# Kernel tuning notes

Measured on AMD Instinct MI355X. Metric: run time of the kernel, lower is better.

The kernel has to match this reference:

```python
import jax, jax.numpy as jnp
import numpy as np

B, S, E = 4, 2048, 1024
H = 16
D = E // H  # head_dim = 64


def setup_inputs() -> dict:
    key = jax.random.key(0)
    k1, k2, k3 = jax.random.split(key, 3)
    x = jax.random.normal(k1, (B, S, E), dtype=jnp.float32)
    w_qkv = jax.random.normal(k2, (E, 3 * E), dtype=jnp.float32) * (E ** -0.5)
    b_qkv = jnp.zeros((3 * E,), dtype=jnp.float32)
    w_proj = jax.random.normal(k3, (E, E), dtype=jnp.float32) * (E ** -0.5)
    b_proj = jnp.zeros((E,), dtype=jnp.float32)
    return {"x": x, "w_qkv": w_qkv, "b_qkv": b_qkv, "w_proj": w_proj, "b_proj": b_proj}


def reference(x, w_qkv, b_qkv, w_proj, b_proj):
    bsz, seq_len, emb = x.shape
    scale = D ** -0.5
    qkv = x @ w_qkv + b_qkv                      # [B,S,3E]
    q, k, v = jnp.split(qkv, 3, axis=2)
    # [B,S,E] -> [B,H,S,D]
    q = q.reshape(bsz, seq_len, H, D).transpose(0, 2, 1, 3)
    k = k.reshape(bsz, seq_len, H, D).transpose(0, 2, 1, 3)
    v = v.reshape(bsz, seq_len, H, D).transpose(0, 2, 1, 3)
    att = jnp.einsum('bhqd,bhkd->bhqk', q, k) * scale
    causal = jnp.tril(jnp.ones((seq_len, seq_len), dtype=bool))
    att = jnp.where(causal, att, -jnp.inf)
    att = jax.nn.softmax(att, axis=-1)
    y = jnp.einsum('bhqk,bhkd->bhqd', att, v)
    y = y.transpose(0, 2, 1, 3).reshape(bsz, seq_len, emb)
    return y @ w_proj + b_proj
```

## Files before the change

### kernel.cpp

```cpp
#include <hip/hip_runtime.h>
#include <hip/hip_bf16.h>
#include <stdint.h>

#define S_LEN 2048
#define EMB   1024
#define NH    16
#define HD    64

typedef unsigned short u16;
typedef __attribute__((ext_vector_type(2))) float f32x2;
typedef __attribute__((ext_vector_type(4))) float f32x4;
typedef __attribute__((ext_vector_type(8))) short bf16x8;

typedef __attribute__((address_space(1))) const unsigned char gas_t;
typedef __attribute__((address_space(3))) unsigned char las_t;

static __device__ __forceinline__ void gld_lds16(const void* g, void* l) {
  __builtin_amdgcn_global_load_lds((gas_t*)g, (las_t*)l, 16, 0, 0);
}

static __device__ __forceinline__ u16 f2bf(float f) {
  unsigned int u = __builtin_bit_cast(unsigned int, f);
  u = u + 0x7fffu + ((u >> 16) & 1u);
  return (u16)(u >> 16);
}

static __device__ __forceinline__ float fexp2(float x) {
  float r;
  asm("v_exp_f32 %0, %1" : "=v"(r) : "v"(x));
  return r;
}

static __device__ __forceinline__ unsigned cvt_pk_bf16(float lo, float hi) {
  unsigned r;
  asm("v_cvt_pk_bf16_f32 %0, %1, %2" : "=v"(r) : "v"(lo), "v"(hi));
  return r;
}

static __device__ __forceinline__ float max3(float a, float b, float c) {
  float r;
  asm("v_max3_f32 %0, %1, %2, %3" : "=v"(r) : "v"(a), "v"(b), "v"(c));
  return r;
}

static __device__ __forceinline__ f32x2 pk_add(f32x2 a, f32x2 b) {
  f32x2 r;
  asm("v_pk_add_f32 %0, %1, %2" : "=v"(r) : "v"(a), "v"(b));
  return r;
}
static __device__ __forceinline__ f32x2 pk_mul(f32x2 a, f32x2 b) {
  f32x2 r;
  asm("v_pk_mul_f32 %0, %1, %2" : "=v"(r) : "v"(a), "v"(b));
  return r;
}
static __device__ __forceinline__ f32x2 pk_fma(f32x2 a, f32x2 b, f32x2 c) {
  f32x2 r;
  asm("v_pk_fma_f32 %0, %1, %2, %3" : "=v"(r) : "v"(a), "v"(b), "v"(c));
  return r;
}
#define HALF0(v) __builtin_shufflevector(v, v, 0, 1)
#define HALF1(v) __builtin_shufflevector(v, v, 2, 3)

static __device__ __forceinline__ float red4rows_max(float x) {
  unsigned u = __builtin_bit_cast(unsigned, x);
  auto r = __builtin_amdgcn_permlane32_swap(u, u, false, false);
  float y = fmaxf(__builtin_bit_cast(float, (unsigned)r[0]),
                  __builtin_bit_cast(float, (unsigned)r[1]));
  unsigned v = __builtin_bit_cast(unsigned, y);
  auto r2 = __builtin_amdgcn_permlane16_swap(v, v, false, false);
  return fmaxf(__builtin_bit_cast(float, (unsigned)r2[0]),
               __builtin_bit_cast(float, (unsigned)r2[1]));
}
static __device__ __forceinline__ float red4rows_sum(float x) {
  unsigned u = __builtin_bit_cast(unsigned, x);
  auto r = __builtin_amdgcn_permlane32_swap(u, u, false, false);
  float y = __builtin_bit_cast(float, (unsigned)r[0]) +
            __builtin_bit_cast(float, (unsigned)r[1]);
  unsigned v = __builtin_bit_cast(unsigned, y);
  auto r2 = __builtin_amdgcn_permlane16_swap(v, v, false, false);
  return __builtin_bit_cast(float, (unsigned)r2[0]) +
         __builtin_bit_cast(float, (unsigned)r2[1]);
}

__global__ __launch_bounds__(256) void k_prep(const float* __restrict__ x,
                                              u16* __restrict__ xb,
                                              const float* __restrict__ w_qkv,
                                              u16* __restrict__ wqkvT,
                                              const float* __restrict__ w_proj,
                                              u16* __restrict__ wprojT) {
  __shared__ u16 tile[64][68];
  const int bid = blockIdx.x;
  const int t = threadIdx.x;
  if (bid < 1024) {
    const int n4 = (8192 * 1024) / 4;
    int i = bid * 256 + t;
    for (; i < n4; i += 1024 * 256) {
      float4 f = ((const float4*)x)[i];
      ushort4 o;
      o.x = f2bf(f.x); o.y = f2bf(f.y); o.z = f2bf(f.z); o.w = f2bf(f.w);
      ((ushort4*)xb)[i] = o;
    }
    return;
  }
  const float* W;
  u16* WT;
  int c0, r0, K, N;
  if (bid < 1792) {
    const int idx = bid - 1024;
    W = w_qkv; WT = wqkvT; K = 1024; N = 3072;
    c0 = (idx % 48) * 64; r0 = (idx / 48) * 64;
  } else {
    const int idx = bid - 1792;
    W = w_proj; WT = wprojT; K = 1024; N = 1024;
    c0 = (idx & 15) * 64; r0 = (idx >> 4) * 64;
  }
  const int tr = t >> 4, tc4 = (t & 15) * 4;
#pragma unroll
  for (int i = 0; i < 4; i++) {
    const int r = tr + 16 * i;
    float4 f = *(const float4*)&W[(size_t)(r0 + r) * N + c0 + tc4];
    ushort4 o;
    o.x = f2bf(f.x); o.y = f2bf(f.y); o.z = f2bf(f.z); o.w = f2bf(f.w);
    *(ushort4*)&tile[r][tc4] = o;
  }
  __syncthreads();
  const int oc = t >> 2, or0 = (t & 3) * 16;
  u16 vals[16];
#pragma unroll
  for (int j = 0; j < 16; j++) vals[j] = tile[or0 + j][oc];
  u16* dst = &WT[(size_t)(c0 + oc) * K + r0 + or0];
  *(uint4*)dst = *(const uint4*)&vals[0];
  *(uint4*)(dst + 8) = *(const uint4*)&vals[8];
}

template <int MODE>
__global__ __launch_bounds__(256) void k_gemm(const u16* __restrict__ A,
                                              const u16* __restrict__ BT,
                                              const float* __restrict__ bias,
                                              float* __restrict__ Cout,
                                              u16* __restrict__ q_ws,
                                              u16* __restrict__ k_ws,
                                              u16* __restrict__ v_t,
                                              int N, int K) {
  __shared__ u16 As[2][128 * 32];
  __shared__ u16 Bs[2][128 * 32];
  const int tid = threadIdx.x;
  const int w = tid >> 6, lane = tid & 63;
  const int wr = w >> 1, wc = w & 1;
  const int lrow = lane & 15, lk8 = (lane >> 4) * 8;
  const int orig = blockIdx.y * gridDim.x + blockIdx.x;
  const int total = gridDim.x * gridDim.y;
  const int wgid = (orig & 7) * (total >> 3) + (orig >> 3);
  const int bxn = wgid % gridDim.x;
  const int byn = wgid / gridDim.x;
  const int brow = byn * 128, bcol = bxn * 128;
  const int srow = lane >> 2;
  const int scol = (lane & 3) * 8;

  const f32x4 zero = {0.f, 0.f, 0.f, 0.f};
  f32x4 acc[4][4];
#pragma unroll
  for (int m = 0; m < 4; m++)
#pragma unroll
    for (int n = 0; n < 4; n++) acc[m][n] = zero;

  auto stage = [&](int kt, int buf) {
#pragma unroll
    for (int i = 0; i < 2; i++) {
      const int c = w * 2 + i;
      const int row = c * 16 + srow;
      gld_lds16(&A[(size_t)(brow + row) * K + kt + scol], (void*)(&As[buf][c * 512]));
      gld_lds16(&BT[(size_t)(bcol + row) * K + kt + scol], (void*)(&Bs[buf][c * 512]));
    }
  };

  const int NK = K >> 5;
  stage(0, 0);
  __syncthreads();
  for (int it = 0; it < NK; ++it) {
    const int cur = it & 1;
    if (it + 1 < NK) stage((it + 1) << 5, cur ^ 1);
    bf16x8 af[4], bfr[4];
#pragma unroll
    for (int mt = 0; mt < 4; mt++)
      af[mt] = *(const bf16x8*)&As[cur][(wr * 64 + mt * 16 + lrow) * 32 + lk8];
#pragma unroll
    for (int nt = 0; nt < 4; nt++)
      bfr[nt] = *(const bf16x8*)&Bs[cur][(wc * 64 + nt * 16 + lrow) * 32 + lk8];
#pragma unroll
    for (int mt = 0; mt < 4; mt++)
#pragma unroll
      for (int nt = 0; nt < 4; nt++)
        acc[mt][nt] = __builtin_amdgcn_mfma_f32_16x16x32_bf16(af[mt], bfr[nt],
                                                              acc[mt][nt], 0, 0, 0);
    __syncthreads();
  }

  if constexpr (MODE == 0) {
    const int which = bcol >> 10;
#pragma unroll
    for (int mt = 0; mt < 4; mt++)
#pragma unroll
      for (int nt = 0; nt < 4; nt++) {
        const int col = bcol + wc * 64 + nt * 16 + lrow;
        const int e = col & 1023;
        const int h = e >> 6, d = e & 63;
        const int row0 = brow + wr * 64 + mt * 16 + (lane >> 4) * 4;
        const int b = row0 >> 11, s0 = row0 & 2047;
        const size_t bh = (size_t)(b * NH + h);
        const float bv = bias[col];
        if (which == 2) {
          ushort4 pk;
          pk.x = f2bf(acc[mt][nt][0] + bv);
          pk.y = f2bf(acc[mt][nt][1] + bv);
          pk.z = f2bf(acc[mt][nt][2] + bv);
          pk.w = f2bf(acc[mt][nt][3] + bv);
          *(ushort4*)&v_t[(bh * HD + d) * S_LEN + s0] = pk;
        } else {
          u16* dst = which ? k_ws : q_ws;
#pragma unroll
          for (int r = 0; r < 4; r++)
            dst[(bh * S_LEN + s0 + r) * HD + d] = f2bf(acc[mt][nt][r] + bv);
        }
      }
  } else {
#pragma unroll
    for (int mt = 0; mt < 4; mt++)
#pragma unroll
      for (int nt = 0; nt < 4; nt++)
#pragma unroll
        for (int r = 0; r < 4; r++) {
          const int row = brow + wr * 64 + mt * 16 + (lane >> 4) * 4 + r;
          const int col = bcol + wc * 64 + nt * 16 + lrow;
          Cout[(size_t)row * N + col] = acc[mt][nt][r] + bias[col];
        }
  }
}

__global__ __launch_bounds__(256, 2) void k_attn(const u16* __restrict__ q_ws,
                                                 const u16* __restrict__ k_ws,
                                                 const u16* __restrict__ v_t,
                                                 u16* __restrict__ y) {
  __shared__ u16 Kl[2][64 * 64];
  __shared__ u16 Vl[2][64 * 64];
  const int tid = threadIdx.x;
  const int w = tid >> 6, lane = tid & 63;
  const int lrow = lane & 15, lk8 = (lane >> 4) * 8;
  const int g4 = (lane >> 4) * 4;
  const int mthr = w * 16 + lrow - g4;
  const int f = blockIdx.y * 16 + blockIdx.x;
  const int pr = (f >> 3) & 15;
  const int bh = (f & 7) + ((f >> 7) << 3);
  const int tileA = pr, tileB = 31 - pr;
  const size_t base = (size_t)bh * S_LEN * HD;
  const float SC = 0.125f * 1.4426950408889634f;

  bf16x8 qfA[2], qfB[2];
#pragma unroll
  for (int ks = 0; ks < 2; ks++) {
    qfA[ks] = *(const bf16x8*)&q_ws[base + (size_t)(tileA * 64 + w * 16 + lrow) * HD + ks * 32 + lk8];
    qfB[ks] = *(const bf16x8*)&q_ws[base + (size_t)(tileB * 64 + w * 16 + lrow) * HD + ks * 32 + lk8];
  }

  const f32x4 zero = {0.f, 0.f, 0.f, 0.f};
  f32x4 oA[4], oB[4];
#pragma unroll
  for (int dt = 0; dt < 4; dt++) { oA[dt] = zero; oB[dt] = zero; }
  float mA = -1e30f, lA = 0.f, mB = -1e30f, lB = 0.f;

  auto stage = [&](int jb, int buf) {
#pragma unroll
    for (int i = 0; i < 2; i++) {
      const int c = w * 2 + i;
      const int row = c * 8 + (lane >> 3);
      const int blk = (lane & 7) ^ (row & 7);
      gld_lds16(&k_ws[base + (size_t)(jb * 64 + row) * HD + blk * 8],
                (void*)(&Kl[buf][c * 512]));
      gld_lds16(&v_t[base + (size_t)row * S_LEN + jb * 64 + blk * 8],
                (void*)(&Vl[buf][c * 512]));
    }
  };

  auto qk = [&](const bf16x8 (&kf)[2][4], const bf16x8 (&qf)[2], f32x4 (&sa)[4]) {
#pragma unroll
    for (int nt = 0; nt < 4; nt++) sa[nt] = zero;
#pragma unroll
    for (int ks = 0; ks < 2; ks++)
#pragma unroll
      for (int nt = 0; nt < 4; nt++)
        sa[nt] = __builtin_amdgcn_mfma_f32_16x16x32_bf16(kf[ks][nt], qf[ks], sa[nt], 0, 0, 0);
  };

  auto softmax = [&](f32x4 (&sa)[4], f32x4 (&o)[4], float& m_run, float& l_run,
                     bool maskDiag, bf16x8 (&pfrag)[2]) {
    if (maskDiag) {
#pragma unroll
      for (int nt = 0; nt < 4; nt++)
#pragma unroll
        for (int r = 0; r < 4; r++)
          if (nt * 16 + r > mthr) sa[nt][r] = -3.0e38f;
    }

    const float m0 = max3(sa[0][0], sa[0][1], sa[0][2]);
    const float m1 = max3(sa[0][3], sa[1][0], sa[1][1]);
    const float m2 = max3(sa[1][2], sa[1][3], sa[2][0]);
    const float m3 = max3(sa[2][1], sa[2][2], sa[2][3]);
    const float m4 = max3(sa[3][0], sa[3][1], sa[3][2]);
    const float m5 = max3(m0, m1, m2);
    const float m6 = max3(m3, m4, sa[3][3]);
    float mx = fmaxf(m5, m6);
    mx = red4rows_max(mx);
    const float mxs = mx * SC;
    const bool nogrow = __all(mxs <= m_run + 8.0f);
    float mn = m_run;
    if (!nogrow) {
      mn = fmaxf(m_run, mxs);
      const float alpha = fexp2(m_run - mn);
      l_run *= alpha;
      const f32x2 al2 = {alpha, alpha};
#pragma unroll
      for (int dt = 0; dt < 4; dt++)
        o[dt] = __builtin_shufflevector(pk_mul(HALF0(o[dt]), al2),
                                        pk_mul(HALF1(o[dt]), al2), 0, 1, 2, 3);
      m_run = mn;
    }
    const f32x2 scv = {SC, SC};
    const f32x2 nm2 = {-mn, -mn};
    f32x2 p2[4][2];
#pragma unroll
    for (int nt = 0; nt < 4; nt++) {
      const f32x2 t0 = pk_fma(HALF0(sa[nt]), scv, nm2);
      const f32x2 t1 = pk_fma(HALF1(sa[nt]), scv, nm2);
      f32x2 p0; p0[0] = fexp2(t0[0]); p0[1] = fexp2(t0[1]);
      f32x2 p1; p1[0] = fexp2(t1[0]); p1[1] = fexp2(t1[1]);
      p2[nt][0] = p0;
      p2[nt][1] = p1;
    }
    f32x2 s0 = pk_add(p2[0][0], p2[0][1]);
    f32x2 s1 = pk_add(p2[1][0], p2[1][1]);
    f32x2 s2 = pk_add(p2[2][0], p2[2][1]);
    f32x2 s3 = pk_add(p2[3][0], p2[3][1]);
    s0 = pk_add(s0, s1);
    s2 = pk_add(s2, s3);
    s0 = pk_add(s0, s2);
    float sum = s0[0] + s0[1];
    sum = red4rows_sum(sum);
    l_run += sum;

    unsigned pk[4][2];
#pragma unroll
    for (int nt = 0; nt < 4; nt++) {
      pk[nt][0] = cvt_pk_bf16(p2[nt][0][0], p2[nt][0][1]);
      pk[nt][1] = cvt_pk_bf16(p2[nt][1][0], p2[nt][1][1]);
    }
    union { unsigned u[4]; bf16x8 v; } c0, c1;
    {
      auto r0 = __builtin_amdgcn_permlane32_swap(pk[0][0], pk[1][0], false, false);
      auto s0p = __builtin_amdgcn_permlane16_swap(r0[0], r0[1], false, false);
      auto r1 = __builtin_amdgcn_permlane32_swap(pk[0][1], pk[1][1], false, false);
      auto s1p = __builtin_amdgcn_permlane16_swap(r1[0], r1[1], false, false);
      c0.u[0] = s0p[0]; c0.u[1] = s1p[0]; c0.u[2] = s0p[1]; c0.u[3] = s1p[1];
      auto r2 = __builtin_amdgcn_permlane32_swap(pk[2][0], pk[3][0], false, false);
      auto s2p = __builtin_amdgcn_permlane16_swap(r2[0], r2[1], false, false);
      auto r3 = __builtin_amdgcn_permlane32_swap(pk[2][1], pk[3][1], false, false);
      auto s3p = __builtin_amdgcn_permlane16_swap(r3[0], r3[1], false, false);
      c1.u[0] = s2p[0]; c1.u[1] = s3p[0]; c1.u[2] = s2p[1]; c1.u[3] = s3p[1];
    }
    pfrag[0] = c0.v;
    pfrag[1] = c1.v;
  };

  stage(0, 0);
  __syncthreads();
  for (int jb = 0; jb <= tileB; jb++) {
    const int cur = jb & 1;
    if (jb < tileB) stage(jb + 1, cur ^ 1);
    const bool doA = (jb <= tileA);

    bf16x8 kf[2][4];
#pragma unroll
    for (int ks = 0; ks < 2; ks++)
#pragma unroll
      for (int nt = 0; nt < 4; nt++) {
        const int kvr = nt * 16 + lrow;
        const int blk = (ks * 4 + (lane >> 4)) ^ (kvr & 7);
        kf[ks][nt] = *(const bf16x8*)&Kl[cur][kvr * 64 + blk * 8];
      }
    f32x4 saB[4], saA[4];
    __builtin_amdgcn_s_setprio(1);
    qk(kf, qfB, saB);
    if (doA) qk(kf, qfA, saA);
    __builtin_amdgcn_s_setprio(0);

    bf16x8 vf[2][4];
#pragma unroll
    for (int ks = 0; ks < 2; ks++)
#pragma unroll
      for (int dt = 0; dt < 4; dt++) {
        const int vr = dt * 16 + lrow;
        const int vblk = (ks * 4 + (lane >> 4)) ^ (vr & 7);
        vf[ks][dt] = *(const bf16x8*)&Vl[cur][vr * 64 + vblk * 8];
      }

    bf16x8 pfB[2], pfA[2];
    softmax(saB, oB, mB, lB, jb == tileB, pfB);
    if (doA) softmax(saA, oA, mA, lA, jb == tileA, pfA);

    __builtin_amdgcn_s_setprio(1);
#pragma unroll
    for (int ks = 0; ks < 2; ks++)
#pragma unroll
      for (int dt = 0; dt < 4; dt++)
        oB[dt] = __builtin_amdgcn_mfma_f32_16x16x32_bf16(vf[ks][dt], pfB[ks], oB[dt], 0, 0, 0);
    if (doA) {
#pragma unroll
      for (int ks = 0; ks < 2; ks++)
#pragma unroll
        for (int dt = 0; dt < 4; dt++)
          oA[dt] = __builtin_amdgcn_mfma_f32_16x16x32_bf16(vf[ks][dt], pfA[ks], oA[dt], 0, 0, 0);
    }
    __builtin_amdgcn_s_setprio(0);
    __syncthreads();
  }

  const int b = bh >> 4, h = bh & 15;
  const float invA = 1.0f / lA;
  const float invB = 1.0f / lB;
  const int qgA = tileA * 64 + w * 16 + lrow;
  const int qgB = tileB * 64 + w * 16 + lrow;
#pragma unroll
  for (int dt = 0; dt < 4; dt++) {
    uint2 pa, pb;
    pa.x = cvt_pk_bf16(oA[dt][0] * invA, oA[dt][1] * invA);
    pa.y = cvt_pk_bf16(oA[dt][2] * invA, oA[dt][3] * invA);
    pb.x = cvt_pk_bf16(oB[dt][0] * invB, oB[dt][1] * invB);
    pb.y = cvt_pk_bf16(oB[dt][2] * invB, oB[dt][3] * invB);
    *(uint2*)&y[(size_t)(b * S_LEN + qgA) * EMB + h * HD + dt * 16 + g4] = pa;
    *(uint2*)&y[(size_t)(b * S_LEN + qgB) * EMB + h * HD + dt * 16 + g4] = pb;
  }
}

extern "C" void kernel_launch(void* const* d_in, const int* in_sizes, int n_in,
                              void* d_out, int out_size, void* d_ws, size_t ws_size,
                              hipStream_t stream) {
  const float* x      = (const float*)d_in[0];
  const float* w_qkv  = (const float*)d_in[1];
  const float* b_qkv  = (const float*)d_in[2];
  const float* w_proj = (const float*)d_in[3];
  const float* b_proj = (const float*)d_in[4];
  float* out = (float*)d_out;

  char* ws = (char*)d_ws;
  u16* wqkvT  = (u16*)(ws);
  u16* wprojT = (u16*)(ws + 6291456);
  u16* xb     = (u16*)(ws + 8388608);
  u16* q_ws   = (u16*)(ws + 25165824);
  u16* k_ws   = (u16*)(ws + 41943040);
  u16* v_t    = (u16*)(ws + 58720256);
  u16* y_att  = xb;

  k_prep<<<dim3(2048), dim3(256), 0, stream>>>(x, xb, w_qkv, wqkvT, w_proj, wprojT);
  k_gemm<0><<<dim3(24, 64), dim3(256), 0, stream>>>(xb, wqkvT, b_qkv, nullptr,
                                                    q_ws, k_ws, v_t, 3072, 1024);
  k_attn<<<dim3(16, 64), dim3(256), 0, stream>>>(q_ws, k_ws, v_t, y_att);
  k_gemm<1><<<dim3(8, 64), dim3(256), 0, stream>>>(y_att, wprojT, b_proj, out,
                                                   nullptr, nullptr, nullptr, 1024, 1024);
}
```

Before: 182.4 us.

## Use 128-row query tiles with 8 waves per attention block

The attention kernel now runs 512-thread blocks, each handling a pair of 128-row query tiles instead of 64-row tiles, with each wave owning 16 query rows. Every staged 64-key K/V tile is therefore shared by twice as many queries, which halves the global and LDS staging traffic per query. Per-wave causal skipping and diagonal masking are worked out from key offsets. The cost is a grid half the size, more waves idling near the diagonal while still hitting every barrier, and a launch bound that asks for four 512-thread blocks, which may restrict registers.

Result: slower. 281.7 us (+54.4%).

```diff
diff --git a/kernel.cpp b/kernel.cpp
--- a/kernel.cpp
+++ b/kernel.cpp
@@ -237,7 +237,7 @@
   }
 }
 
-__global__ __launch_bounds__(256, 2) void k_attn(const u16* __restrict__ q_ws,
+__global__ __launch_bounds__(512, 4) void k_attn(const u16* __restrict__ q_ws,
                                                  const u16* __restrict__ k_ws,
                                                  const u16* __restrict__ v_t,
                                                  u16* __restrict__ y) {
@@ -247,19 +247,20 @@
   const int w = tid >> 6, lane = tid & 63;
   const int lrow = lane & 15, lk8 = (lane >> 4) * 8;
   const int g4 = (lane >> 4) * 4;
-  const int mthr = w * 16 + lrow - g4;
-  const int f = blockIdx.y * 16 + blockIdx.x;
-  const int pr = (f >> 3) & 15;
-  const int bh = (f & 7) + ((f >> 7) << 3);
-  const int tileA = pr, tileB = 31 - pr;
+  const int wq = w * 16;
+  const int mthr0 = wq + lrow - g4;
+  const int f = blockIdx.y * 8 + blockIdx.x;
+  const int pr = (f >> 3) & 7;
+  const int bh = (f & 7) + ((f >> 6) << 3);
+  const int tA = pr, tB = 15 - pr;
   const size_t base = (size_t)bh * S_LEN * HD;
   const float SC = 0.125f * 1.4426950408889634f;
 
   bf16x8 qfA[2], qfB[2];
 #pragma unroll
   for (int ks = 0; ks < 2; ks++) {
-    qfA[ks] = *(const bf16x8*)&q_ws[base + (size_t)(tileA * 64 + w * 16 + lrow) * HD + ks * 32 + lk8];
-    qfB[ks] = *(const bf16x8*)&q_ws[base + (size_t)(tileB * 64 + w * 16 + lrow) * HD + ks * 32 + lk8];
+    qfA[ks] = *(const bf16x8*)&q_ws[base + (size_t)(tA * 128 + wq + lrow) * HD + ks * 32 + lk8];
+    qfB[ks] = *(const bf16x8*)&q_ws[base + (size_t)(tB * 128 + wq + lrow) * HD + ks * 32 + lk8];
   }
 
   const f32x4 zero = {0.f, 0.f, 0.f, 0.f};
@@ -269,16 +270,12 @@
   float mA = -1e30f, lA = 0.f, mB = -1e30f, lB = 0.f;
 
   auto stage = [&](int jb, int buf) {
-#pragma unroll
-    for (int i = 0; i < 2; i++) {
-      const int c = w * 2 + i;
-      const int row = c * 8 + (lane >> 3);
-      const int blk = (lane & 7) ^ (row & 7);
-      gld_lds16(&k_ws[base + (size_t)(jb * 64 + row) * HD + blk * 8],
-                (void*)(&Kl[buf][c * 512]));
-      gld_lds16(&v_t[base + (size_t)row * S_LEN + jb * 64 + blk * 8],
-                (void*)(&Vl[buf][c * 512]));
-    }
+    const int row = w * 8 + (lane >> 3);
+    const int blk = (lane & 7) ^ (row & 7);
+    gld_lds16(&k_ws[base + (size_t)(jb * 64 + row) * HD + blk * 8],
+              (void*)(&Kl[buf][w * 512]));
+    gld_lds16(&v_t[base + (size_t)row * S_LEN + jb * 64 + blk * 8],
+              (void*)(&Vl[buf][w * 512]));
   };
 
   auto qk = [&](const bf16x8 (&kf)[2][4], const bf16x8 (&qf)[2], f32x4 (&sa)[4]) {
@@ -292,7 +289,7 @@
   };
 
   auto softmax = [&](f32x4 (&sa)[4], f32x4 (&o)[4], float& m_run, float& l_run,
-                     bool maskDiag, bf16x8 (&pfrag)[2]) {
+                     bool maskDiag, int mthr, bf16x8 (&pfrag)[2]) {
     if (maskDiag) {
 #pragma unroll
       for (int nt = 0; nt < 4; nt++)
@@ -370,64 +367,73 @@
     pfrag[1] = c1.v;
   };
 
+  const int NT = 2 * tB + 2;
   stage(0, 0);
   __syncthreads();
-  for (int jb = 0; jb <= tileB; jb++) {
+  for (int jb = 0; jb < NT; jb++) {
     const int cur = jb & 1;
-    if (jb < tileB) stage(jb + 1, cur ^ 1);
-    const bool doA = (jb <= tileA);
-
-    bf16x8 kf[2][4];
-#pragma unroll
-    for (int ks = 0; ks < 2; ks++)
-#pragma unroll
-      for (int nt = 0; nt < 4; nt++) {
-        const int kvr = nt * 16 + lrow;
-        const int blk = (ks * 4 + (lane >> 4)) ^ (kvr & 7);
-        kf[ks][nt] = *(const bf16x8*)&Kl[cur][kvr * 64 + blk * 8];
+    if (jb + 1 < NT) stage(jb + 1, cur ^ 1);
+
+    const int kvoffB = jb * 64 - tB * 128;
+    const int kvoffA = jb * 64 - tA * 128;
+    const bool doB = (kvoffB <= wq + 15);
+    const bool doA = (jb <= 2 * tA + 1) && (kvoffA <= wq + 15);
+
+    if (doB || doA) {
+      bf16x8 kf[2][4];
+#pragma unroll
+      for (int ks = 0; ks < 2; ks++)
+#pragma unroll
+        for (int nt = 0; nt < 4; nt++) {
+          const int kvr = nt * 16 + lrow;
+          const int blk = (ks * 4 + (lane >> 4)) ^ (kvr & 7);
+          kf[ks][nt] = *(const bf16x8*)&Kl[cur][kvr * 64 + blk * 8];
+        }
+      f32x4 saB[4], saA[4];
+      __builtin_amdgcn_s_setprio(1);
+      if (doB) qk(kf, qfB, saB);
+      if (doA) qk(kf, qfA, saA);
+      __builtin_amdgcn_s_setprio(0);
+
+      bf16x8 vf[2][4];
+#pragma unroll
+      for (int ks = 0; ks < 2; ks++)
+#pragma unroll
+        for (int dt = 0; dt < 4; dt++) {
+          const int vr = dt * 16 + lrow;
+          const int vblk = (ks * 4 + (lane >> 4)) ^ (vr & 7);
+          vf[ks][dt] = *(const bf16x8*)&Vl[cur][vr * 64 + vblk * 8];
+        }
+
+      bf16x8 pfB[2], pfA[2];
+      if (doB) softmax(saB, oB, mB, lB, kvoffB + 63 > wq, mthr0 - kvoffB, pfB);
+      if (doA) softmax(saA, oA, mA, lA, kvoffA + 63 > wq, mthr0 - kvoffA, pfA);
+
+      __builtin_amdgcn_s_setprio(1);
+      if (doB) {
+#pragma unroll
+        for (int ks = 0; ks < 2; ks++)
+#pragma unroll
+          for (int dt = 0; dt < 4; dt++)
+            oB[dt] = __builtin_amdgcn_mfma_f32_16x16x32_bf16(vf[ks][dt], pfB[ks], oB[dt], 0, 0, 0);
       }
-    f32x4 saB[4], saA[4];
-    __builtin_amdgcn_s_setprio(1);
-    qk(kf, qfB, saB);
-    if (doA) qk(kf, qfA, saA);
-    __builtin_amdgcn_s_setprio(0);
-
-    bf16x8 vf[2][4];
-#pragma unroll
-    for (int ks = 0; ks < 2; ks++)
-#pragma unroll
-      for (int dt = 0; dt < 4; dt++) {
-        const int vr = dt * 16 + lrow;
-        const int vblk = (ks * 4 + (lane >> 4)) ^ (vr & 7);
-        vf[ks][dt] = *(const bf16x8*)&Vl[cur][vr * 64 + vblk * 8];
+      if (doA) {
+#pragma unroll
+        for (int ks = 0; ks < 2; ks++)
+#pragma unroll
+          for (int dt = 0; dt < 4; dt++)
+            oA[dt] = __builtin_amdgcn_mfma_f32_16x16x32_bf16(vf[ks][dt], pfA[ks], oA[dt], 0, 0, 0);
       }
-
-    bf16x8 pfB[2], pfA[2];
-    softmax(saB, oB, mB, lB, jb == tileB, pfB);
-    if (doA) softmax(saA, oA, mA, lA, jb == tileA, pfA);
-
-    __builtin_amdgcn_s_setprio(1);
-#pragma unroll
-    for (int ks = 0; ks < 2; ks++)
-#pragma unroll
-      for (int dt = 0; dt < 4; dt++)
-        oB[dt] = __builtin_amdgcn_mfma_f32_16x16x32_bf16(vf[ks][dt], pfB[ks], oB[dt], 0, 0, 0);
-    if (doA) {
-#pragma unroll
-      for (int ks = 0; ks < 2; ks++)
-#pragma unroll
-        for (int dt = 0; dt < 4; dt++)
-          oA[dt] = __builtin_amdgcn_mfma_f32_16x16x32_bf16(vf[ks][dt], pfA[ks], oA[dt], 0, 0, 0);
-    }
-    __builtin_amdgcn_s_setprio(0);
+      __builtin_amdgcn_s_setprio(0);
+    }
     __syncthreads();
   }
 
   const int b = bh >> 4, h = bh & 15;
   const float invA = 1.0f / lA;
   const float invB = 1.0f / lB;
-  const int qgA = tileA * 64 + w * 16 + lrow;
-  const int qgB = tileB * 64 + w * 16 + lrow;
+  const int qgA = tA * 128 + wq + lrow;
+  const int qgB = tB * 128 + wq + lrow;
 #pragma unroll
   for (int dt = 0; dt < 4; dt++) {
     uint2 pa, pb;
@@ -462,7 +468,7 @@
   k_prep<<<dim3(2048), dim3(256), 0, stream>>>(x, xb, w_qkv, wqkvT, w_proj, wprojT);
   k_gemm<0><<<dim3(24, 64), dim3(256), 0, stream>>>(xb, wqkvT, b_qkv, nullptr,
                                                     q_ws, k_ws, v_t, 3072, 1024);
-  k_attn<<<dim3(16, 64), dim3(256), 0, stream>>>(q_ws, k_ws, v_t, y_att);
+  k_attn<<<dim3(8, 64), dim3(512), 0, stream>>>(q_ws, k_ws, v_t, y_att);
   k_gemm<1><<<dim3(8, 64), dim3(256), 0, stream>>>(y_att, wprojT, b_proj, out,
                                                    nullptr, nullptr, nullptr, 1024, 1024);
 }
```
